# Kernel optimization log

Measured on AMD Instinct MI355X. Metric: run time of the kernel, lower is better.

## Reference

```python
import jax, jax.numpy as jnp
import numpy as np

NUM_GRAPHS = 128
N_NODES = 50000
N_EDGES = 400000
EMB = 384
L = 5
BN_EPS = 1e-5


def _bn(h, gamma, beta):
    # training-mode BatchNorm1d over the node/edge dim (biased variance, like torch)
    m = h.mean(axis=0)
    v = h.var(axis=0)
    return gamma * (h - m) * jax.lax.rsqrt(v + BN_EPS) + beta


def setup_inputs() -> dict:
    key = jax.random.key(0)
    ks = jax.random.split(key, 16)
    batch = jnp.sort(jax.random.randint(ks[0], (N_NODES,), 0, NUM_GRAPHS))
    x = jax.random.randint(ks[1], (N_NODES, 9), 0, 64)
    edge_index = jax.random.randint(ks[2], (2, N_EDGES), 0, N_NODES)
    edge_attr = jax.random.randint(ks[3], (N_EDGES, 3), 0, 8)
    s = 0.05
    atom_emb = jax.random.normal(ks[4], (9, 64, EMB), jnp.float32) * s
    bond_emb = jax.random.normal(ks[5], (3, 8, EMB), jnp.float32) * s
    # per-layer GINE MLP params, stacked over layers
    W1 = jax.random.normal(ks[6], (L, EMB, 2 * EMB), jnp.float32) * (1.0 / np.sqrt(EMB))
    b1 = jnp.zeros((L, 2 * EMB), jnp.float32)
    g1 = jnp.ones((L, 2 * EMB), jnp.float32)
    be1 = jnp.zeros((L, 2 * EMB), jnp.float32)
    W2 = jax.random.normal(ks[7], (L, 2 * EMB, EMB), jnp.float32) * (1.0 / np.sqrt(2 * EMB))
    b2 = jnp.zeros((L, EMB), jnp.float32)
    # outer per-layer BatchNorm params
    gbn = jnp.ones((L, EMB), jnp.float32)
    bbn = jnp.zeros((L, EMB), jnp.float32)
    return {"batch": batch, "x": x, "edge_index": edge_index, "edge_attr": edge_attr,
            "atom_emb": atom_emb, "bond_emb": bond_emb,
            "W1": W1, "b1": b1, "g1": g1, "be1": be1,
            "W2": W2, "b2": b2, "gbn": gbn, "bbn": bbn}


def reference(batch, x, edge_index, edge_attr, atom_emb, bond_emb,
              W1, b1, g1, be1, W2, b2, gbn, bbn):
    # AtomEncoder / BondEncoder: sum of per-column embedding lookups
    h = atom_emb[jnp.arange(9), x].sum(axis=1)          # [N, EMB]
    e = bond_emb[jnp.arange(3), edge_attr].sum(axis=1)  # [E, EMB]
    src, dst = edge_index[0], edge_index[1]
    for i in range(W1.shape[0]):
        # GINEConv: sum_j relu(x_j + e_ij)  (edge_weight defaults to ones)
        msg = jax.nn.relu(h[src] + e)                                   # [E, EMB]
        agg = jax.ops.segment_sum(msg, dst, num_segments=N_NODES)      # [N, EMB]
        z = h + agg                                                     # (1+eps)*x_i + agg, eps=0
        # MLP: Linear -> BN -> ReLU -> Linear
        z = z @ W1[i] + b1[i]
        z = jax.nn.relu(_bn(z, g1[i], be1[i]))
        z = z @ W2[i] + b2[i]
        # outer BN + ReLU (drop_ratio = 0.0)
        h = jax.nn.relu(_bn(z, gbn[i], bbn[i]))
    # standard pooling: global_add_pool
    graph_emb = jax.ops.segment_sum(h, batch, num_segments=NUM_GRAPHS)  # [G, EMB]
    return graph_emb, h
```

## Files before the change

kernel.cpp:

```cpp
#include <hip/hip_runtime.h>
#include <stdint.h>

#define NN 50000
#define NE 400000
#define EMB 384
#define NH 768
#define NL 5

typedef __bf16 bf16x8_t __attribute__((ext_vector_type(8)));
typedef float  f32x4_t  __attribute__((ext_vector_type(4)));

__device__ __forceinline__ float bflo(uint32_t u){ union{uint32_t u;float f;} v; v.u = u<<16; return v.f; }
__device__ __forceinline__ float bfhi(uint32_t u){ union{uint32_t u;float f;} v; v.u = u & 0xffff0000u; return v.f; }
__device__ __forceinline__ uint16_t f2bf(float f){
  union{float f;uint32_t u;} v; v.f=f;
  uint32_t r = v.u + 0x7fffu + ((v.u>>16)&1u);
  return (uint16_t)(r>>16);
}
__device__ __forceinline__ uint32_t bfpack2(float a, float b){
  return (uint32_t)f2bf(a) | ((uint32_t)f2bf(b)<<16);
}

__device__ __forceinline__ void gld16(uint16_t* ldsp, const uint16_t* gp){
  __builtin_amdgcn_global_load_lds(
      (const __attribute__((address_space(1))) uint32_t*)gp,
      (__attribute__((address_space(3))) uint32_t*)ldsp,
      16, 0, 0);
}

__global__ void hist_kernel(const int* __restrict__ dst, int* __restrict__ count){
  int i = blockIdx.x*256 + threadIdx.x;
  if (i < NE) atomicAdd(&count[dst[i]], 1);
}
__global__ void scan_block_sum(const int* __restrict__ count, int* __restrict__ bsum, int n){
  __shared__ int s[256];
  int i = blockIdx.x*256 + threadIdx.x;
  s[threadIdx.x] = (i<n) ? count[i] : 0;
  __syncthreads();
  for (int st=128; st>0; st>>=1){
    if (threadIdx.x < st) s[threadIdx.x] += s[threadIdx.x+st];
    __syncthreads();
  }
  if (threadIdx.x==0) bsum[blockIdx.x] = s[0];
}
__global__ void scan_excl_small(int* __restrict__ bsum, int nb){
  __shared__ int s[256];
  int t = threadIdx.x;
  int v = (t<nb) ? bsum[t] : 0;
  s[t] = v;
  __syncthreads();
  for (int st=1; st<256; st<<=1){
    int u = (t>=st) ? s[t-st] : 0;
    __syncthreads();
    s[t] += u;
    __syncthreads();
  }
  if (t<nb) bsum[t] = s[t] - v;
}
__global__ void scan_final(const int* __restrict__ count, const int* __restrict__ bsum,
                           int* __restrict__ rowptr, int* __restrict__ cursor, int n){
  __shared__ int s[256];
  int t = threadIdx.x;
  int i = blockIdx.x*256 + t;
  int v = (i<n) ? count[i] : 0;
  s[t] = v;
  __syncthreads();
  for (int st=1; st<256; st<<=1){
    int u = (t>=st) ? s[t-st] : 0;
    __syncthreads();
    s[t] += u;
    __syncthreads();
  }
  int off = bsum[blockIdx.x] + s[t] - v;
  if (i < n){
    rowptr[i] = off; cursor[i] = off;
    if (i == n-1) rowptr[n] = off + v;
  }
}
__global__ void scatter_kernel(const int* __restrict__ dst, const int* __restrict__ src,
                               const int* __restrict__ eattr, int* __restrict__ cursor,
                               int* __restrict__ csr_src, int* __restrict__ csr_code){
  int e = blockIdx.x*256 + threadIdx.x;
  if (e < NE){
    int p = atomicAdd(&cursor[dst[e]], 1);
    csr_src[p] = src[e];
    csr_code[p] = eattr[e*3] | (eattr[e*3+1]<<3) | (eattr[e*3+2]<<6);
  }
}

__global__ void build_bond(const float* __restrict__ bemb, uint16_t* __restrict__ bt){
  const int code = blockIdx.x;
  const int t0 = code&7, t1=(code>>3)&7, t2=code>>6;
  const int c = threadIdx.x;
  const float2 a = ((const float2*)(bemb + (size_t)( 0+t0)*EMB))[c];
  const float2 b = ((const float2*)(bemb + (size_t)( 8+t1)*EMB))[c];
  const float2 d = ((const float2*)(bemb + (size_t)(16+t2)*EMB))[c];
  ((uint32_t*)(bt + (size_t)code*EMB))[c] = bfpack2(a.x+b.x+d.x, a.y+b.y+d.y);
}

__global__ void transpose_w(const float* __restrict__ in, uint16_t* __restrict__ outp,
                            int R, int Cc){
  __shared__ float tile[32][33];
  const size_t lo = (size_t)blockIdx.z * R * Cc;
  int cb = blockIdx.x*32, rb = blockIdx.y*32;
  int r = rb + threadIdx.y, c = cb + threadIdx.x;
  if (r < R && c < Cc) tile[threadIdx.y][threadIdx.x] = in[lo + (size_t)r*Cc + c];
  __syncthreads();
  int orr = cb + threadIdx.y, occ = rb + threadIdx.x;
  if (orr < Cc && occ < R) outp[lo + (size_t)orr*R + occ] = f2bf(tile[threadIdx.x][threadIdx.y]);
}

__global__ __launch_bounds__(256) void atom_encode(
    const int* __restrict__ x, const float* __restrict__ aemb,
    uint16_t* __restrict__ h){
  const int w = threadIdx.x >> 6, lane = threadIdx.x & 63;
  const int i = blockIdx.x*4 + w;
  if (i >= NN) return;
  float a0=0,a1=0,a2=0,a3=0,a4=0,a5=0;
  #pragma unroll
  for (int k=0;k<9;k++){
    const int idx = x[i*9+k];
    const float2* p = (const float2*)(aemb + ((size_t)(k*64+idx))*EMB) + lane*3;
    float2 u0=p[0], u1=p[1], u2=p[2];
    a0+=u0.x; a1+=u0.y; a2+=u1.x; a3+=u1.y; a4+=u2.x; a5+=u2.y;
  }
  uint32_t* hp = (uint32_t*)(h + (size_t)i*EMB) + lane*3;
  hp[0]=bfpack2(a0,a1); hp[1]=bfpack2(a2,a3); hp[2]=bfpack2(a4,a5);
}

template<int BNREL>
__global__ __launch_bounds__(256) void agg_kernel(
    const uint16_t* __restrict__ in, const uint16_t* __restrict__ bondt,
    const float* __restrict__ scale, const float* __restrict__ shift,
    const int* __restrict__ rowptr, const int* __restrict__ csr_src,
    const int* __restrict__ csr_code, uint16_t* __restrict__ za){
  const int w = threadIdx.x >> 6, lane = threadIdx.x & 63;
  const int i = blockIdx.x*4 + w;
  if (i >= NN) return;

  float sc0=0,sc1=0,sc2=0,sc3=0,sc4=0,sc5=0, sh0=0,sh1=0,sh2=0,sh3=0,sh4=0,sh5=0;
  if (BNREL){
    const int c = lane*6;
    sc0=scale[c]; sc1=scale[c+1]; sc2=scale[c+2]; sc3=scale[c+3]; sc4=scale[c+4]; sc5=scale[c+5];
    sh0=shift[c]; sh1=shift[c+1]; sh2=shift[c+2]; sh3=shift[c+3]; sh4=shift[c+4]; sh5=shift[c+5];
  }

  const uint32_t* hs = (const uint32_t*)(in + (size_t)i*EMB) + lane*3;
  uint32_t s0=hs[0], s1=hs[1], s2=hs[2];
  float a0,a1,a2,a3,a4,a5;
  if (BNREL){
    a0 = fmaxf(bflo(s0)*sc0+sh0, 0.f); a1 = fmaxf(bfhi(s0)*sc1+sh1, 0.f);
    a2 = fmaxf(bflo(s1)*sc2+sh2, 0.f); a3 = fmaxf(bfhi(s1)*sc3+sh3, 0.f);
    a4 = fmaxf(bflo(s2)*sc4+sh4, 0.f); a5 = fmaxf(bfhi(s2)*sc5+sh5, 0.f);
  } else {
    a0 = bflo(s0); a1 = bfhi(s0); a2 = bflo(s1); a3 = bfhi(s1); a4 = bflo(s2); a5 = bfhi(s2);
  }

  const int rs = rowptr[i], re = rowptr[i+1];
  int k = rs;
  for (; k + 4 <= re; k += 4){
    int sj[4], cj[4];
    #pragma unroll
    for (int j=0;j<4;j++){ sj[j]=csr_src[k+j]; cj[j]=csr_code[k+j]; }
    uint32_t u[4][3], b[4][3];
    #pragma unroll
    for (int j=0;j<4;j++){
      const uint32_t* hp = (const uint32_t*)(in + (size_t)sj[j]*EMB) + lane*3;
      u[j][0]=hp[0]; u[j][1]=hp[1]; u[j][2]=hp[2];
      const uint32_t* bp = (const uint32_t*)(bondt + (size_t)cj[j]*EMB) + lane*3;
      b[j][0]=bp[0]; b[j][1]=bp[1]; b[j][2]=bp[2];
    }
    #pragma unroll
    for (int j=0;j<4;j++){
      float v0,v1,v2,v3,v4,v5;
      if (BNREL){
        v0 = fmaxf(bflo(u[j][0])*sc0+sh0, 0.f); v1 = fmaxf(bfhi(u[j][0])*sc1+sh1, 0.f);
        v2 = fmaxf(bflo(u[j][1])*sc2+sh2, 0.f); v3 = fmaxf(bfhi(u[j][1])*sc3+sh3, 0.f);
        v4 = fmaxf(bflo(u[j][2])*sc4+sh4, 0.f); v5 = fmaxf(bfhi(u[j][2])*sc5+sh5, 0.f);
      } else {
        v0=bflo(u[j][0]); v1=bfhi(u[j][0]); v2=bflo(u[j][1]);
        v3=bfhi(u[j][1]); v4=bflo(u[j][2]); v5=bfhi(u[j][2]);
      }
      a0 += fmaxf(v0+bflo(b[j][0]), 0.f); a1 += fmaxf(v1+bfhi(b[j][0]), 0.f);
      a2 += fmaxf(v2+bflo(b[j][1]), 0.f); a3 += fmaxf(v3+bfhi(b[j][1]), 0.f);
      a4 += fmaxf(v4+bflo(b[j][2]), 0.f); a5 += fmaxf(v5+bfhi(b[j][2]), 0.f);
    }
  }
  for (; k < re; k++){
    const int s = csr_src[k];
    const int code = csr_code[k];
    const uint32_t* hp = (const uint32_t*)(in + (size_t)s*EMB) + lane*3;
    uint32_t u0=hp[0], u1=hp[1], u2=hp[2];
    const uint32_t* bp = (const uint32_t*)(bondt + (size_t)code*EMB) + lane*3;
    uint32_t b0=bp[0], b1=bp[1], b2=bp[2];
    float v0,v1,v2,v3,v4,v5;
    if (BNREL){
      v0 = fmaxf(bflo(u0)*sc0+sh0, 0.f); v1 = fmaxf(bfhi(u0)*sc1+sh1, 0.f);
      v2 = fmaxf(bflo(u1)*sc2+sh2, 0.f); v3 = fmaxf(bfhi(u1)*sc3+sh3, 0.f);
      v4 = fmaxf(bflo(u2)*sc4+sh4, 0.f); v5 = fmaxf(bfhi(u2)*sc5+sh5, 0.f);
    } else {
      v0=bflo(u0); v1=bfhi(u0); v2=bflo(u1); v3=bfhi(u1); v4=bflo(u2); v5=bfhi(u2);
    }
    a0 += fmaxf(v0+bflo(b0), 0.f); a1 += fmaxf(v1+bfhi(b0), 0.f);
    a2 += fmaxf(v2+bflo(b1), 0.f); a3 += fmaxf(v3+bfhi(b1), 0.f);
    a4 += fmaxf(v4+bflo(b2), 0.f); a5 += fmaxf(v5+bfhi(b2), 0.f);
  }

  uint32_t* zp = (uint32_t*)(za + (size_t)i*EMB) + lane*3;
  zp[0] = bfpack2(a0,a1);
  zp[1] = bfpack2(a2,a3);
  zp[2] = bfpack2(a4,a5);
}

template<int BNA>
__global__ __launch_bounds__(256) void gemm_bt(
    const uint16_t* __restrict__ A, const uint16_t* __restrict__ Bt,
    const float* __restrict__ bias, const float* __restrict__ scA,
    const float* __restrict__ shA, uint16_t* __restrict__ C,
    float* __restrict__ stats, int M, int N, int K, int nbr){
  __shared__ __align__(16) uint16_t As[2][128*32];
  __shared__ __align__(16) uint16_t Bs[2][128*32];
  __shared__ float sAs[BNA ? NH : 1];
  __shared__ float hAs[BNA ? NH : 1];
  __shared__ float csum[128];
  __shared__ float csq[128];

  const int tid = threadIdx.x;
  const int nbc = N >> 7;
  const int xcd = blockIdx.x & 7;
  const int slot = blockIdx.x >> 3;
  const int bcol = slot % nbc;
  const int brow = (slot / nbc)*8 + xcd;
  if (brow >= nbr) return;
  const int rowbase = brow << 7;

  const int lane = tid & 63;
  const int w = tid >> 6;
  const int wm = w >> 1, wn = w & 1;
  const int quad = lane >> 4, l16 = lane & 15;

  const int s0 = tid, s1 = 256 + tid;
  const int kq0 = s0 >> 7, r0 = s0 & 127;
  const int kq1 = s1 >> 7, r1 = s1 & 127;
  int gra0 = rowbase + r0; if (gra0 >= M) gra0 = M-1;
  int gra1 = rowbase + r1; if (gra1 >= M) gra1 = M-1;
  const int pb0 = bcol*128 + (r0 & 64) + ((r0 & 15) << 2) + ((r0 >> 4) & 3);
  const int pb1 = bcol*128 + (r1 & 64) + ((r1 & 15) << 2) + ((r1 >> 4) & 3);

  const uint16_t* gA0 = A + (size_t)gra0*K + kq0*8;
  const uint16_t* gA1 = A + (size_t)gra1*K + kq1*8;
  const uint16_t* gB0 = Bt + (size_t)pb0*K + kq0*8;
  const uint16_t* gB1 = Bt + (size_t)pb1*K + kq1*8;

  f32x4_t acc[4][4];
  #pragma unroll
  for (int mi=0;mi<4;mi++)
    #pragma unroll
    for (int ni=0;ni<4;ni++)
      acc[mi][ni] = (f32x4_t){0.f,0.f,0.f,0.f};

  auto stageB = [&](int buf, int kk){
    gld16(&Bs[buf][s0*8], gB0 + kk);
    gld16(&Bs[buf][s1*8], gB1 + kk);
  };
  auto stageA_dma = [&](int buf, int kk){
    gld16(&As[buf][s0*8], gA0 + kk);
    gld16(&As[buf][s1*8], gA1 + kk);
  };
  auto stageA_bn = [&](int buf, int kk, uint4 va, uint4 vb){
    uint32_t in0[4] = {va.x,va.y,va.z,va.w};
    uint32_t in1[4] = {vb.x,vb.y,vb.z,vb.w};
    uint32_t o0[4], o1[4];
    const int kb0 = kk + kq0*8, kb1 = kk + kq1*8;
    #pragma unroll
    for (int j=0;j<4;j++){
      float x0 = fmaxf(bflo(in0[j])*sAs[kb0+2*j  ]+hAs[kb0+2*j  ], 0.f);
      float x1 = fmaxf(bfhi(in0[j])*sAs[kb0+2*j+1]+hAs[kb0+2*j+1], 0.f);
      o0[j] = bfpack2(x0,x1);
      float y0 = fmaxf(bflo(in1[j])*sAs[kb1+2*j  ]+hAs[kb1+2*j  ], 0.f);
      float y1 = fmaxf(bfhi(in1[j])*sAs[kb1+2*j+1]+hAs[kb1+2*j+1], 0.f);
      o1[j] = bfpack2(y0,y1);
    }
    *(uint4*)&As[buf][s0*8] = make_uint4(o0[0],o0[1],o0[2],o0[3]);
    *(uint4*)&As[buf][s1*8] = make_uint4(o1[0],o1[1],o1[2],o1[3]);
  };
  auto compute = [&](int buf){
    bf16x8_t fa[4], fb[4];
    #pragma unroll
    for (int mi=0;mi<4;mi++)
      fa[mi] = *(const bf16x8_t*)&As[buf][(quad*128 + wm*64 + mi*16 + l16)*8];
    #pragma unroll
    for (int ni=0;ni<4;ni++)
      fb[ni] = *(const bf16x8_t*)&Bs[buf][(quad*128 + wn*64 + ni*16 + l16)*8];
    #pragma unroll
    for (int mi=0;mi<4;mi++)
      #pragma unroll
      for (int ni=0;ni<4;ni++)
        acc[mi][ni] = __builtin_amdgcn_mfma_f32_16x16x32_bf16(fa[mi], fb[ni], acc[mi][ni], 0,0,0);
  };

  const int nk = K >> 5;

  uint4 pa0{}, pa1{}, qa0{}, qa1{};
  if (BNA){
    for (int i = tid; i < K; i += 256){ sAs[i] = scA[i]; hAs[i] = shA[i]; }
    pa0 = *(const uint4*)(gA0);      pa1 = *(const uint4*)(gA1);
    qa0 = *(const uint4*)(gA0 + 32); qa1 = *(const uint4*)(gA1 + 32);
    __syncthreads();
    stageA_bn(0, 0, pa0, pa1);
    if (nk > 2){ pa0 = *(const uint4*)(gA0 + 64); pa1 = *(const uint4*)(gA1 + 64); }
  } else {
    stageA_dma(0, 0);
  }
  stageB(0, 0);
  __syncthreads();

  int cur = 0;
  for (int ks = 0; ks < nk; ks += 2){
    {
      const int nx = cur ^ 1;
      if (ks + 1 < nk){
        stageB(nx, (ks+1)*32);
        if (BNA) stageA_bn(nx, (ks+1)*32, qa0, qa1);
        else     stageA_dma(nx, (ks+1)*32);
      }
      if (BNA && ks + 3 < nk){
        qa0 = *(const uint4*)(gA0 + (ks+3)*32);
        qa1 = *(const uint4*)(gA1 + (ks+3)*32);
      }
      compute(cur);
      __syncthreads();
      cur = nx;
    }
    {
      const int nx = cur ^ 1;
      if (ks + 2 < nk){
        stageB(nx, (ks+2)*32);
        if (BNA) stageA_bn(nx, (ks+2)*32, pa0, pa1);
        else     stageA_dma(nx, (ks+2)*32);
      }
      if (BNA && ks + 4 < nk){
        pa0 = *(const uint4*)(gA0 + (ks+4)*32);
        pa1 = *(const uint4*)(gA1 + (ks+4)*32);
      }
      compute(cur);
      __syncthreads();
      cur = nx;
    }
  }

  if (tid < 128){ csum[tid]=0.f; csq[tid]=0.f; }
  __syncthreads();

  const int lcol = wn*64 + l16*4;
  const int colbase = bcol*128 + lcol;
  float bv[4], ssum[4] = {0,0,0,0}, sq[4] = {0,0,0,0};
  #pragma unroll
  for (int ni=0;ni<4;ni++) bv[ni] = bias[colbase + ni];

  #pragma unroll
  for (int mi=0;mi<4;mi++){
    #pragma unroll
    for (int r=0;r<4;r++){
      const int grow = rowbase + wm*64 + mi*16 + quad*4 + r;
      if (grow < M){
        float v0 = acc[mi][0][r] + bv[0];
        float v1 = acc[mi][1][r] + bv[1];
        float v2 = acc[mi][2][r] + bv[2];
        float v3 = acc[mi][3][r] + bv[3];
        uint2 pk = make_uint2(bfpack2(v0,v1), bfpack2(v2,v3));
        *(uint2*)(C + (size_t)grow*N + colbase) = pk;
        ssum[0]+=v0; ssum[1]+=v1; ssum[2]+=v2; ssum[3]+=v3;
        sq[0]+=v0*v0; sq[1]+=v1*v1; sq[2]+=v2*v2; sq[3]+=v3*v3;
      }
    }
  }
  #pragma unroll
  for (int ni=0;ni<4;ni++){
    ssum[ni] += __shfl_xor(ssum[ni], 16); ssum[ni] += __shfl_xor(ssum[ni], 32);
    sq[ni]   += __shfl_xor(sq[ni],   16); sq[ni]   += __shfl_xor(sq[ni],   32);
  }
  if (quad == 0){
    #pragma unroll
    for (int ni=0;ni<4;ni++){
      atomicAdd(&csum[lcol + ni], ssum[ni]);
      atomicAdd(&csq [lcol + ni], sq[ni]);
    }
  }
  __syncthreads();
  if (tid < 128){
    atomicAdd(&stats[bcol*128 + tid], csum[tid]);
    atomicAdd(&stats[N + bcol*128 + tid], csq[tid]);
  }
}

__global__ void bn_finalize(float* __restrict__ stats, const float* __restrict__ gamma,
                            const float* __restrict__ beta, float* __restrict__ scale,
                            float* __restrict__ shift, int n, float invM){
  int c = blockIdx.x*256 + threadIdx.x;
  if (c < n){
    float mean = stats[c]*invM;
    float var  = stats[n+c]*invM - mean*mean;
    float sc = gamma[c] * rsqrtf(var + 1e-5f);
    scale[c] = sc;
    shift[c] = beta[c] - mean*sc;
    stats[c] = 0.f;
    stats[n+c] = 0.f;
  }
}

__global__ void bn_relu_final(const uint16_t* __restrict__ u, const float* __restrict__ scale,
                              const float* __restrict__ shift, float* __restrict__ hf){
  int i = blockIdx.x*256 + threadIdx.x;
  const int total2 = NN*EMB/2;
  if (i >= total2) return;
  uint32_t v = ((const uint32_t*)u)[i];
  int c = (i*2) % EMB;
  float f0 = fmaxf(bflo(v)*scale[c  ] + shift[c  ], 0.f);
  float f1 = fmaxf(bfhi(v)*scale[c+1] + shift[c+1], 0.f);
  ((float2*)hf)[i] = make_float2(f0, f1);
}

__global__ void pool_kernel(const float* __restrict__ h, const int* __restrict__ batch,
                            float* __restrict__ pool){
  __shared__ int bs[64];
  int c = threadIdx.x;
  int n0 = blockIdx.x*64;
  if (c < 64){ int i = n0 + c; bs[c] = (i < NN) ? batch[i] : -1; }
  __syncthreads();
  float sum = 0.f; int cur = -1;
  for (int tt=0; tt<64; tt++){
    int i = n0 + tt;
    if (i >= NN) break;
    int g = bs[tt];
    float v = h[(size_t)i*EMB + c];
    if (g != cur){
      if (cur >= 0) atomicAdd(&pool[(size_t)cur*EMB + c], sum);
      cur = g; sum = v;
    } else sum += v;
  }
  if (cur >= 0) atomicAdd(&pool[(size_t)cur*EMB + c], sum);
}
__global__ void pool_to_out(const float* __restrict__ pool, float* __restrict__ outp){
  int i = blockIdx.x*256 + threadIdx.x;
  if (i < 128*EMB) outp[i] = pool[i];
}

extern "C" void kernel_launch(void* const* d_in, const int* in_sizes, int n_in,
                              void* d_out, int out_size, void* d_ws, size_t ws_size,
                              hipStream_t stream){
  (void)in_sizes; (void)n_in; (void)out_size; (void)ws_size;
  const int* batch = (const int*)d_in[0];
  const int* x     = (const int*)d_in[1];
  const int* eidx  = (const int*)d_in[2];
  const int* eattr = (const int*)d_in[3];
  const float* aemb = (const float*)d_in[4];
  const float* bemb = (const float*)d_in[5];
  const float* W1 = (const float*)d_in[6];
  const float* b1 = (const float*)d_in[7];
  const float* g1 = (const float*)d_in[8];
  const float* be1= (const float*)d_in[9];
  const float* W2 = (const float*)d_in[10];
  const float* b2 = (const float*)d_in[11];
  const float* gbn= (const float*)d_in[12];
  const float* bbn= (const float*)d_in[13];
  float* out = (float*)d_out;

  char* base = (char*)d_ws;
  size_t off = 0;
  auto alloc = [&](size_t bytes) -> void* {
    void* p = base + off;
    off = (off + bytes + 255) & ~(size_t)255;
    return p;
  };
  uint16_t* za   = (uint16_t*)alloc((size_t)NN*EMB*2);
  uint16_t* zm   = (uint16_t*)alloc((size_t)NN*EMB*2);
  uint16_t* t    = (uint16_t*)alloc((size_t)NN*NH*2);
  uint16_t* W1t  = (uint16_t*)alloc((size_t)NL*NH*EMB*2);
  uint16_t* W2t  = (uint16_t*)alloc((size_t)NL*EMB*NH*2);
  uint16_t* bondt= (uint16_t*)alloc((size_t)512*EMB*2);
  float* stats1  = (float*)alloc(NH*2*4);
  float* stats2  = (float*)alloc(EMB*2*4);
  float* scale1  = (float*)alloc(NH*4);
  float* shift1  = (float*)alloc(NH*4);
  float* scale2  = (float*)alloc(EMB*4);
  float* shift2  = (float*)alloc(EMB*4);
  float* pool    = (float*)alloc(128*EMB*4);
  int* count   = (int*)alloc((size_t)NN*4);
  int* rowptr  = (int*)alloc((size_t)(NN+1)*4);
  int* cursor  = (int*)alloc((size_t)NN*4);
  int* bsum    = (int*)alloc(256*4);
  int* csr_src = (int*)alloc((size_t)NE*4);
  int* csr_code= (int*)alloc((size_t)NE*4);

  const int* esrc = eidx;
  const int* edst = eidx + NE;
  const int nsb = (NN + 255)/256;

  hipMemsetAsync(count, 0, (size_t)NN*4, stream);
  hist_kernel<<<(NE+255)/256, 256, 0, stream>>>(edst, count);
  scan_block_sum<<<nsb, 256, 0, stream>>>(count, bsum, NN);
  scan_excl_small<<<1, 256, 0, stream>>>(bsum, nsb);
  scan_final<<<nsb, 256, 0, stream>>>(count, bsum, rowptr, cursor, NN);
  scatter_kernel<<<(NE+255)/256, 256, 0, stream>>>(edst, esrc, eattr, cursor, csr_src, csr_code);

  build_bond<<<512, 192, 0, stream>>>(bemb, bondt);
  transpose_w<<<dim3(NH/32, EMB/32, NL), dim3(32,32), 0, stream>>>(W1, W1t, EMB, NH);
  transpose_w<<<dim3(EMB/32, NH/32, NL), dim3(32,32), 0, stream>>>(W2, W2t, NH, EMB);

  atom_encode<<<NN/4, 256, 0, stream>>>(x, aemb, zm);
  hipMemsetAsync(pool, 0, (size_t)128*EMB*4, stream);
  hipMemsetAsync(stats1, 0, (size_t)(6144 + 3072), stream);

  const int nbr = (NN + 127)/128;
  const int nbrr = ((nbr + 7)/8)*8;
  const int g1blocks = nbrr*(NH/128);
  const int g2blocks = nbrr*(EMB/128);
  for (int l = 0; l < NL; l++){
    if (l == 0)
      agg_kernel<0><<<NN/4, 256, 0, stream>>>(zm, bondt, nullptr, nullptr,
                                              rowptr, csr_src, csr_code, za);
    else
      agg_kernel<1><<<NN/4, 256, 0, stream>>>(zm, bondt, scale2, shift2,
                                              rowptr, csr_src, csr_code, za);
    gemm_bt<0><<<g1blocks, 256, 0, stream>>>(
        za, W1t + (size_t)l*NH*EMB, b1 + l*NH, nullptr, nullptr, t, stats1, NN, NH, EMB, nbr);
    bn_finalize<<<(NH+255)/256, 256, 0, stream>>>(stats1, g1 + l*NH, be1 + l*NH,
                                                  scale1, shift1, NH, 1.0f/NN);
    gemm_bt<1><<<g2blocks, 256, 0, stream>>>(
        t, W2t + (size_t)l*EMB*NH, b2 + l*EMB, scale1, shift1, zm, stats2, NN, EMB, NH, nbr);
    bn_finalize<<<(EMB+255)/256, 256, 0, stream>>>(stats2, gbn + l*EMB, bbn + l*EMB,
                                                   scale2, shift2, EMB, 1.0f/NN);
  }
  bn_relu_final<<<(NN*EMB/2 + 255)/256, 256, 0, stream>>>(zm, scale2, shift2, out + 128*EMB);
  pool_kernel<<<(NN+63)/64, 384, 0, stream>>>(out + 128*EMB, batch, pool);
  pool_to_out<<<(128*EMB+255)/256, 256, 0, stream>>>(pool, out);
}
```

Measured before the change: 1.320 ms.

## Triple-buffer GEMM LDS tiles with explicit vmcnt waits and single barrier per step

Restructures the GEMM main loop from a two-buffer ping-pong into a three-stage pipeline. Loads for tile t+2 are issued while tile t is computed, using manual s_waitcnt vmcnt and one s_barrier per k-step. The loop is unrolled by 6 so the mod-3 and mod-2 buffer indices stay static. The goal is to hide global-to-LDS latency and cut barrier count, at the cost of more LDS and fragile hand-tuned wait counts. The loop assumes nk is a multiple of 6, which holds for K=384 and K=768.

```diff
diff --git a/kernel.cpp b/kernel.cpp
--- a/kernel.cpp
+++ b/kernel.cpp
@@ -218,8 +218,8 @@
     const float* __restrict__ bias, const float* __restrict__ scA,
     const float* __restrict__ shA, uint16_t* __restrict__ C,
     float* __restrict__ stats, int M, int N, int K, int nbr){
-  __shared__ __align__(16) uint16_t As[2][128*32];
-  __shared__ __align__(16) uint16_t Bs[2][128*32];
+  __shared__ __align__(16) uint16_t As[BNA ? 2 : 3][128*32];
+  __shared__ __align__(16) uint16_t Bs[3][128*32];
   __shared__ float sAs[BNA ? NH : 1];
   __shared__ float hAs[BNA ? NH : 1];
   __shared__ float csum[128];
@@ -259,15 +259,7 @@
     for (int ni=0;ni<4;ni++)
       acc[mi][ni] = (f32x4_t){0.f,0.f,0.f,0.f};
 
-  auto stageB = [&](int buf, int kk){
-    gld16(&Bs[buf][s0*8], gB0 + kk);
-    gld16(&Bs[buf][s1*8], gB1 + kk);
-  };
-  auto stageA_dma = [&](int buf, int kk){
-    gld16(&As[buf][s0*8], gA0 + kk);
-    gld16(&As[buf][s1*8], gA1 + kk);
-  };
-  auto stageA_bn = [&](int buf, int kk, uint4 va, uint4 vb){
+  auto stageA_bn = [&](int pi, int kk, uint4 va, uint4 vb){
     uint32_t in0[4] = {va.x,va.y,va.z,va.w};
     uint32_t in1[4] = {vb.x,vb.y,vb.z,vb.w};
     uint32_t o0[4], o1[4];
@@ -281,17 +273,17 @@
       float y1 = fmaxf(bfhi(in1[j])*sAs[kb1+2*j+1]+hAs[kb1+2*j+1], 0.f);
       o1[j] = bfpack2(y0,y1);
     }
-    *(uint4*)&As[buf][s0*8] = make_uint4(o0[0],o0[1],o0[2],o0[3]);
-    *(uint4*)&As[buf][s1*8] = make_uint4(o1[0],o1[1],o1[2],o1[3]);
+    *(uint4*)&As[pi][s0*8] = make_uint4(o0[0],o0[1],o0[2],o0[3]);
+    *(uint4*)&As[pi][s1*8] = make_uint4(o1[0],o1[1],o1[2],o1[3]);
   };
-  auto compute = [&](int buf){
+  auto computeT = [&](int ai, int bi){
     bf16x8_t fa[4], fb[4];
     #pragma unroll
     for (int mi=0;mi<4;mi++)
-      fa[mi] = *(const bf16x8_t*)&As[buf][(quad*128 + wm*64 + mi*16 + l16)*8];
+      fa[mi] = *(const bf16x8_t*)&As[ai][(quad*128 + wm*64 + mi*16 + l16)*8];
     #pragma unroll
     for (int ni=0;ni<4;ni++)
-      fb[ni] = *(const bf16x8_t*)&Bs[buf][(quad*128 + wn*64 + ni*16 + l16)*8];
+      fb[ni] = *(const bf16x8_t*)&Bs[bi][(quad*128 + wn*64 + ni*16 + l16)*8];
     #pragma unroll
     for (int mi=0;mi<4;mi++)
       #pragma unroll
@@ -301,51 +293,53 @@
 
   const int nk = K >> 5;
 
-  uint4 pa0{}, pa1{}, qa0{}, qa1{};
+  uint4 ar[2][2];
   if (BNA){
     for (int i = tid; i < K; i += 256){ sAs[i] = scA[i]; hAs[i] = shA[i]; }
-    pa0 = *(const uint4*)(gA0);      pa1 = *(const uint4*)(gA1);
-    qa0 = *(const uint4*)(gA0 + 32); qa1 = *(const uint4*)(gA1 + 32);
     __syncthreads();
-    stageA_bn(0, 0, pa0, pa1);
-    if (nk > 2){ pa0 = *(const uint4*)(gA0 + 64); pa1 = *(const uint4*)(gA1 + 64); }
+    ar[0][0] = *(const uint4*)(gA0);
+    ar[0][1] = *(const uint4*)(gA1);
   } else {
-    stageA_dma(0, 0);
-  }
-  stageB(0, 0);
-  __syncthreads();
-
-  int cur = 0;
-  for (int ks = 0; ks < nk; ks += 2){
-    {
-      const int nx = cur ^ 1;
-      if (ks + 1 < nk){
-        stageB(nx, (ks+1)*32);
-        if (BNA) stageA_bn(nx, (ks+1)*32, qa0, qa1);
-        else     stageA_dma(nx, (ks+1)*32);
+    gld16(&As[0][s0*8], gA0);
+    gld16(&As[0][s1*8], gA1);
+  }
+  gld16(&Bs[0][s0*8], gB0);
+  gld16(&Bs[0][s1*8], gB1);
+  __builtin_amdgcn_sched_barrier(0);
+  if (BNA){
+    ar[1][0] = *(const uint4*)(gA0 + 32);
+    ar[1][1] = *(const uint4*)(gA1 + 32);
+  } else {
+    gld16(&As[1][s0*8], gA0 + 32);
+    gld16(&As[1][s1*8], gA1 + 32);
+  }
+  gld16(&Bs[1][s0*8], gB0 + 32);
+  gld16(&Bs[1][s1*8], gB1 + 32);
+
+  for (int base = 0; base < nk; base += 6){
+    #pragma unroll
+    for (int j = 0; j < 6; j++){
+      const int t = base + j;
+      if (t < nk - 1) asm volatile("s_waitcnt vmcnt(4)" ::: "memory");
+      else            asm volatile("s_waitcnt vmcnt(0)" ::: "memory");
+      if (BNA){
+        stageA_bn(j & 1, t*32, ar[j & 1][0], ar[j & 1][1]);
+        asm volatile("s_waitcnt lgkmcnt(0)" ::: "memory");
       }
-      if (BNA && ks + 3 < nk){
-        qa0 = *(const uint4*)(gA0 + (ks+3)*32);
-        qa1 = *(const uint4*)(gA1 + (ks+3)*32);
+      __builtin_amdgcn_s_barrier();
+      __builtin_amdgcn_sched_barrier(0);
+      if (t + 2 < nk){
+        if (BNA){
+          ar[j & 1][0] = *(const uint4*)(gA0 + (t+2)*32);
+          ar[j & 1][1] = *(const uint4*)(gA1 + (t+2)*32);
+        } else {
+          gld16(&As[(j+2)%3][s0*8], gA0 + (t+2)*32);
+          gld16(&As[(j+2)%3][s1*8], gA1 + (t+2)*32);
+        }
+        gld16(&Bs[(j+2)%3][s0*8], gB0 + (t+2)*32);
+        gld16(&Bs[(j+2)%3][s1*8], gB1 + (t+2)*32);
       }
-      compute(cur);
-      __syncthreads();
-      cur = nx;
-    }
-    {
-      const int nx = cur ^ 1;
-      if (ks + 2 < nk){
-        stageB(nx, (ks+2)*32);
-        if (BNA) stageA_bn(nx, (ks+2)*32, pa0, pa1);
-        else     stageA_dma(nx, (ks+2)*32);
-      }
-      if (BNA && ks + 4 < nk){
-        pa0 = *(const uint4*)(gA0 + (ks+4)*32);
-        pa1 = *(const uint4*)(gA1 + (ks+4)*32);
-      }
-      compute(cur);
-      __syncthreads();
-      cur = nx;
+      computeT(BNA ? (j & 1) : (j % 3), j % 3);
     }
   }
 
```

Result: no change. 1.332 ms (+0.9%).
